# Performance work log

Hardware: AMD Instinct MI355X
Metric: run time of the kernel (lower is better)

## Reference

```python
import jax, jax.numpy as jnp
import numpy as np

N = 262144          # nodes
E = N * 16          # edges (avg degree 16)
C_IN = 64
C_OUT = 64
GRID = 0.5          # voxel size
POS_EXTENT = 10.0   # pos in [0, 10)^3
NVOX_DIM = int(round(POS_EXTENT / GRID))  # 20
NVOX = NVOX_DIM ** 3                      # 8000 voxels
BN_EPS = 1e-5


def setup_inputs() -> dict:
    key = jax.random.key(0)
    k = jax.random.split(key, 5)
    x = jax.random.normal(k[0], (N, C_IN), dtype=jnp.float32)
    pos = jax.random.uniform(k[1], (N, 3), dtype=jnp.float32, minval=0.0, maxval=POS_EXTENT)
    edge_index = jax.random.randint(k[2], (2, E), 0, N, dtype=jnp.int32)
    W = jax.random.normal(k[3], (C_IN, C_OUT), dtype=jnp.float32) / np.float32(np.sqrt(C_IN))
    b = jnp.zeros((C_OUT,), jnp.float32)
    gamma = jnp.ones((C_OUT,), jnp.float32)
    beta = jnp.zeros((C_OUT,), jnp.float32)
    return {"x": x, "pos": pos, "edge_index": edge_index,
            "W": W, "b": b, "gamma": gamma, "beta": beta}


def reference(x, pos, edge_index, W, b, gamma, beta):
    # --- self.down: Linear -> BatchNorm1d (training-mode batch stats) -> ReLU ---
    h = x @ W + b                                   # [N, C_OUT]
    mean = jnp.mean(h, axis=0)
    var = jnp.mean(jnp.square(h - mean), axis=0)    # biased variance (torch BN)
    h = (h - mean) * jax.lax.rsqrt(var + BN_EPS) * gamma + beta
    h = jax.nn.relu(h)

    # --- max_pool_neighbor_x: scatter-max of neighbor features (self-loops added) ---
    row, col = edge_index[0], edge_index[1]
    pooled = jax.ops.segment_max(h[row], col, num_segments=N)  # [N, C_OUT]
    h = jnp.maximum(pooled, h)  # self-loop; also fixes -inf for isolated nodes

    # --- GridSampling: voxel-grid quantize + per-voxel mean of x and pos ---
    vid = jnp.clip(jnp.floor(pos / GRID).astype(jnp.int32), 0, NVOX_DIM - 1)  # [N,3]
    vox = (vid[:, 0] * NVOX_DIM + vid[:, 1]) * NVOX_DIM + vid[:, 2]           # [N]
    cnt = jax.ops.segment_sum(jnp.ones((N,), jnp.float32), vox, num_segments=NVOX)
    x_sum = jax.ops.segment_sum(h, vox, num_segments=NVOX)     # [NVOX, C_OUT]
    p_sum = jax.ops.segment_sum(pos, vox, num_segments=NVOX)   # [NVOX, 3]
    denom = jnp.maximum(cnt, 1.0)[:, None]
    x_out = x_sum / denom
    pos_out = p_sum / denom
    # concat features and positions of the downsampled graph: [NVOX, C_OUT+3]
    return jnp.concatenate([x_out, pos_out], axis=1)
```

## Files before the change

kernel.cpp:

```cpp
#include <hip/hip_runtime.h>
#include <hip/hip_fp16.h>

#define NVOX_DIM 20
#define NVOX 8000
#define BN_EPS 1e-5f

#define NBUCK 1024
#define BSHIFT 8
#define NODES_PER_BUCK 256
#define GEMM_BLOCKS 1024
#define XTRA_BLOCKS 64
#define CAP_NEW 8192
#define CAP_OLD 5120
#define VCAP 88
#define CSTRIDE 16
#define VSTRIDE 4

typedef _Float16 f16x8 __attribute__((ext_vector_type(8)));
typedef float f32x4 __attribute__((ext_vector_type(4)));

__device__ __forceinline__ unsigned short f2key(float v) {
    unsigned short hb = __half_as_ushort(__float2half(v));
    unsigned short m = (unsigned short)(0x8000u | (unsigned short)(-(int)(hb >> 15)));
    return (unsigned short)(hb ^ m);
}

__device__ __forceinline__ float key2f(unsigned int k) {
    unsigned short hb = (k & 0x8000u) ? (unsigned short)(k ^ 0x8000u)
                                      : (unsigned short)(0xFFFFu ^ k);
    __half_raw hr;
    hr.x = hb;
    return __half2float((__half)hr);
}

__global__ __launch_bounds__(256) void k_zero(int* __restrict__ p, int n) {
    int i = blockIdx.x * 256 + threadIdx.x;
    if (i < n) p[i] = 0;
}

template <int NEW>
__global__ __launch_bounds__(256) void k0_fused(const float* __restrict__ x,
                                                const float* __restrict__ W,
                                                const float* __restrict__ bias,
                                                unsigned short* __restrict__ h16,
                                                float* __restrict__ partials, int n16,
                                                const int* __restrict__ rows,
                                                const int* __restrict__ cols,
                                                int* __restrict__ cursor,
                                                unsigned int* __restrict__ pairs,
                                                const float* __restrict__ pos,
                                                int* __restrict__ vcursor,
                                                int* __restrict__ vlist,
                                                float4* __restrict__ zero_zone,
                                                int zero_n4) {
    __shared__ float sW[4096];
    __shared__ float red[2][4][64];
    __shared__ int lh[NBUCK];
    __shared__ int lpos[NBUCK];
    const int cap = NEW ? CAP_NEW : CAP_OLD;
    int t = threadIdx.x;
    int bid = blockIdx.x;

    if (bid >= 2 * GEMM_BLOCKS) {
        int zb = bid - 2 * GEMM_BLOCKS;
        if (NEW) {
            int nNodes = n16 * 16;
            for (int nd = zb * 256 + t; nd < nNodes; nd += XTRA_BLOCKS * 256) {
                float px = pos[(size_t)nd * 3 + 0];
                float py = pos[(size_t)nd * 3 + 1];
                float pz = pos[(size_t)nd * 3 + 2];
                int v0 = min(max((int)floorf(px * 2.f), 0), NVOX_DIM - 1);
                int v1 = min(max((int)floorf(py * 2.f), 0), NVOX_DIM - 1);
                int v2 = min(max((int)floorf(pz * 2.f), 0), NVOX_DIM - 1);
                int vox = (v0 * NVOX_DIM + v1) * NVOX_DIM + v2;
                int idx = atomicAdd(&vcursor[vox * VSTRIDE], 1);
                if (idx < VCAP) vlist[vox * VCAP + idx] = nd;
            }
        } else {
            float4 z = {0.f, 0.f, 0.f, 0.f};
            for (int i = zb * 256 + t; i < zero_n4; i += XTRA_BLOCKS * 256) zero_zone[i] = z;
        }
        return;
    }

    if (bid & 1) {
        int bb = bid >> 1;
        for (int j = t; j < NBUCK; j += 256) lh[j] = 0;
        __syncthreads();
        int base = bb * 4096 + t * 16;
        int r[16], c[16];
#pragma unroll
        for (int g4 = 0; g4 < 4; ++g4) {
            int e = base + g4 * 4;
            int4 r4 = *(const int4*)(rows + e);
            int4 c4 = *(const int4*)(cols + e);
            r[g4 * 4 + 0] = r4.x; c[g4 * 4 + 0] = c4.x;
            r[g4 * 4 + 1] = r4.y; c[g4 * 4 + 1] = c4.y;
            r[g4 * 4 + 2] = r4.z; c[g4 * 4 + 2] = c4.z;
            r[g4 * 4 + 3] = r4.w; c[g4 * 4 + 3] = c4.w;
        }
#pragma unroll
        for (int i = 0; i < 16; ++i) atomicAdd(&lh[c[i] >> BSHIFT], 1);
        __syncthreads();
        for (int j = t; j < NBUCK; j += 256)
            lpos[j] = atomicAdd(&cursor[j * (NEW ? CSTRIDE : 1)], lh[j]);
        __syncthreads();
#pragma unroll
        for (int i = 0; i < 16; ++i) {
            int bkt = c[i] >> BSHIFT;
            int idx = atomicAdd(&lpos[bkt], 1);
            if (idx < cap)
                pairs[(size_t)bkt * cap + idx] =
                    ((unsigned int)r[i] << 8) | (unsigned int)(c[i] & (NODES_PER_BUCK - 1));
        }
        return;
    }

    int gb = bid >> 1;
    for (int i = t; i < 4096; i += 256) sW[i] = W[i];
    __syncthreads();
    int lane = t & 63;
    int w = t >> 6;
    int l15 = lane & 15;
    int q = lane >> 4;

    f16x8 bf[4][2];
#pragma unroll
    for (int t4 = 0; t4 < 4; ++t4)
#pragma unroll
        for (int kb = 0; kb < 2; ++kb)
#pragma unroll
            for (int i = 0; i < 8; ++i)
                bf[t4][kb][i] = (_Float16)sW[(kb * 32 + q * 8 + i) * 64 + t4 * 16 + l15];
    float bv[4];
#pragma unroll
    for (int t4 = 0; t4 < 4; ++t4) bv[t4] = bias[t4 * 16 + l15];

    float s[4] = {0.f, 0.f, 0.f, 0.f}, s2[4] = {0.f, 0.f, 0.f, 0.f};

    for (int g = gb * 4 + w; g < n16; g += GEMM_BLOCKS * 4) {
        int row0 = g * 16;
        const float* xp = x + (size_t)(row0 + l15) * 64 + q * 8;
        float4 xa = *(const float4*)(xp);
        float4 xb = *(const float4*)(xp + 4);
        float4 xc = *(const float4*)(xp + 32);
        float4 xd = *(const float4*)(xp + 36);
        f16x8 a0, a1;
        a0[0] = (_Float16)xa.x; a0[1] = (_Float16)xa.y; a0[2] = (_Float16)xa.z; a0[3] = (_Float16)xa.w;
        a0[4] = (_Float16)xb.x; a0[5] = (_Float16)xb.y; a0[6] = (_Float16)xb.z; a0[7] = (_Float16)xb.w;
        a1[0] = (_Float16)xc.x; a1[1] = (_Float16)xc.y; a1[2] = (_Float16)xc.z; a1[3] = (_Float16)xc.w;
        a1[4] = (_Float16)xd.x; a1[5] = (_Float16)xd.y; a1[6] = (_Float16)xd.z; a1[7] = (_Float16)xd.w;

#pragma unroll
        for (int t4 = 0; t4 < 4; ++t4) {
            f32x4 acc = {bv[t4], bv[t4], bv[t4], bv[t4]};
            acc = __builtin_amdgcn_mfma_f32_16x16x32_f16(a0, bf[t4][0], acc, 0, 0, 0);
            acc = __builtin_amdgcn_mfma_f32_16x16x32_f16(a1, bf[t4][1], acc, 0, 0, 0);
            s[t4] += acc[0] + acc[1] + acc[2] + acc[3];
            s2[t4] = fmaf(acc[0], acc[0], s2[t4]);
            s2[t4] = fmaf(acc[1], acc[1], s2[t4]);
            s2[t4] = fmaf(acc[2], acc[2], s2[t4]);
            s2[t4] = fmaf(acc[3], acc[3], s2[t4]);
#pragma unroll
            for (int r = 0; r < 4; ++r) {
                h16[(size_t)(row0 + q * 4 + r) * 64 + t4 * 16 + l15] = f2key(acc[r]);
            }
        }
    }

#pragma unroll
    for (int t4 = 0; t4 < 4; ++t4) {
        s[t4] += __shfl_xor(s[t4], 16, 64);
        s[t4] += __shfl_xor(s[t4], 32, 64);
        s2[t4] += __shfl_xor(s2[t4], 16, 64);
        s2[t4] += __shfl_xor(s2[t4], 32, 64);
    }
    if (lane < 16) {
#pragma unroll
        for (int t4 = 0; t4 < 4; ++t4) {
            red[0][w][t4 * 16 + lane] = s[t4];
            red[1][w][t4 * 16 + lane] = s2[t4];
        }
    }
    __syncthreads();
    if (t < 128) {
        int c = t & 63;
        int which = t >> 6;
        float v = red[which][0][c] + red[which][1][c] + red[which][2][c] + red[which][3][c];
        partials[(size_t)gb * 128 + which * 64 + c] = v;
    }
}

__global__ __launch_bounds__(1024) void k3_finalize(const float* __restrict__ partials,
                                                    const float* __restrict__ gamma,
                                                    const float* __restrict__ beta,
                                                    float* __restrict__ stats2, float invN) {
    __shared__ float red[8][128];
    __shared__ float tot[128];
    int t = threadIdx.x;
    int c = t & 127;
    int g = t >> 7;
    float s = 0.f;
    for (int b = g; b < GEMM_BLOCKS; b += 8) s += partials[(size_t)b * 128 + c];
    red[g][c] = s;
    __syncthreads();
    if (t < 128) {
        float v = 0.f;
#pragma unroll
        for (int g2 = 0; g2 < 8; ++g2) v += red[g2][t];
        tot[t] = v;
    }
    __syncthreads();
    if (t < 64) {
        float mean = tot[t] * invN;
        float var = tot[64 + t] * invN - mean * mean;
        float sc = gamma[t] * rsqrtf(var + BN_EPS);
        stats2[t] = sc;
        stats2[64 + t] = beta[t] - mean * sc;
    }
}

template <int NEW>
__global__ __launch_bounds__(1024) void k_pool(const unsigned int* pairs_,
                                               const int* __restrict__ cursor,
                                               const unsigned short* __restrict__ h16,
                                               const float* __restrict__ pos,
                                               float* __restrict__ stats2,
                                               float* __restrict__ xs,
                                               float* __restrict__ ps,
                                               float* __restrict__ cnt,
                                               unsigned short* pooled16,
                                               const float* __restrict__ partials,
                                               const float* __restrict__ gamma,
                                               const float* __restrict__ beta,
                                               float invN) {
    __shared__ unsigned int tile[NODES_PER_BUCK * 64];
    const int cap = NEW ? CAP_NEW : CAP_OLD;
    int b = blockIdx.x;
    int t = threadIdx.x;

    if (NEW && b == NBUCK) {
        float* fred = (float*)tile;
        float* tot = ((float*)tile) + 1024;
        int c = t & 127;
        int g = t >> 7;
        float s = 0.f;
        for (int pb = g; pb < GEMM_BLOCKS; pb += 8) s += partials[(size_t)pb * 128 + c];
        fred[g * 128 + c] = s;
        __syncthreads();
        if (t < 128) {
            float v = 0.f;
#pragma unroll
            for (int g2 = 0; g2 < 8; ++g2) v += fred[g2 * 128 + t];
            tot[t] = v;
        }
        __syncthreads();
        if (t < 64) {
            float mean = tot[t] * invN;
            float var = tot[64 + t] * invN - mean * mean;
            float sc = gamma[t] * rsqrtf(var + BN_EPS);
            stats2[t] = sc;
            stats2[64 + t] = beta[t] - mean * sc;
        }
        return;
    }

    int lane = t & 63;
    int w = t >> 6;

    const unsigned int* src = (const unsigned int*)(h16 + (size_t)b * (NODES_PER_BUCK * 64));
#pragma unroll
    for (int k = 0; k < 8; ++k) {
        int i = t + k * 1024;
        unsigned int u = src[i];
        tile[2 * i] = u & 0xFFFFu;
        tile[2 * i + 1] = u >> 16;
    }
    __syncthreads();

    int cntE = min(cursor[b * (NEW ? CSTRIDE : 1)], cap);
    int start = b * cap;
    int end = start + cntE;
    int chunk = (cntE + 15) >> 4;
    int cs = start + w * chunk;
    int ce = min(cs + chunk, end);
    for (int j0 = cs; j0 < ce; j0 += 64) {
        int lim = min(64, ce - j0);
        unsigned int pk = (lane < lim) ? pairs_[j0 + lane] : 0u;
        int jj = 0;
        for (; jj + 16 <= lim; jj += 16) {
            unsigned int qv[16];
            unsigned short vv[16];
#pragma unroll
            for (int u = 0; u < 16; ++u)
                qv[u] = (unsigned int)__builtin_amdgcn_readlane((int)pk, jj + u);
#pragma unroll
            for (int u = 0; u < 16; ++u) vv[u] = h16[(size_t)(qv[u] >> 8) * 64 + lane];
#pragma unroll
            for (int u = 0; u < 16; ++u)
                atomicMax(&tile[((qv[u] & 255u) << 6) + lane], (unsigned int)vv[u]);
        }
        for (; jj < lim; ++jj) {
            unsigned int qq = (unsigned int)__builtin_amdgcn_readlane((int)pk, jj);
            unsigned int v = h16[(size_t)(qq >> 8) * 64 + lane];
            atomicMax(&tile[((qq & 255u) << 6) + lane], v);
        }
    }
    __syncthreads();

    if (NEW) {
#pragma unroll
        for (int nl = 0; nl < NODES_PER_BUCK; nl += 16) {
            int node_l = nl + w;
            pooled16[((size_t)((b << BSHIFT) + node_l)) * 64 + lane] =
                (unsigned short)tile[(node_l << 6) + lane];
        }
    } else {
        float scale = stats2[lane];
        float shift = stats2[64 + lane];
#pragma unroll
        for (int nl = 0; nl < NODES_PER_BUCK; nl += 16) {
            int node_l = nl + w;
            int c = (b << BSHIFT) + node_l;
            float px = pos[(size_t)c * 3 + 0];
            float py = pos[(size_t)c * 3 + 1];
            float pz = pos[(size_t)c * 3 + 2];
            int v0 = min(max((int)floorf(px * 2.f), 0), NVOX_DIM - 1);
            int v1 = min(max((int)floorf(py * 2.f), 0), NVOX_DIM - 1);
            int v2 = min(max((int)floorf(pz * 2.f), 0), NVOX_DIM - 1);
            int vox = (v0 * NVOX_DIM + v1) * NVOX_DIM + v2;
            float v = key2f(tile[(node_l << 6) + lane]);
            float val = fmaxf(fmaf(v, scale, shift), 0.f);
            atomicAdd(&xs[(size_t)vox * 64 + lane], val);
            if (lane < 3) atomicAdd(&ps[vox * 3 + lane], lane == 0 ? px : (lane == 1 ? py : pz));
            if (lane == 0) atomicAdd(&cnt[vox], 1.f);
        }
    }
}

__global__ __launch_bounds__(256) void k_vox(const unsigned short* __restrict__ pooled16,
                                             const int* __restrict__ vlist,
                                             const int* __restrict__ vcursor,
                                             const float* __restrict__ pos,
                                             const float* __restrict__ stats2,
                                             float* __restrict__ out) {
    int v = blockIdx.x * 4 + (threadIdx.x >> 6);
    int lane = threadIdx.x & 63;
    int cv = vcursor[v * VSTRIDE];
    int c = min(cv, VCAP);
    float scale = stats2[lane], shift = stats2[64 + lane];
    const int* lst = vlist + (size_t)v * VCAP;
    float s0 = 0.f, s1 = 0.f, s2 = 0.f, s3 = 0.f;
    int i = 0;
    for (; i + 4 <= c; i += 4) {
        int n0 = lst[i], n1 = lst[i + 1], n2 = lst[i + 2], n3 = lst[i + 3];
        float v0 = key2f(pooled16[(size_t)n0 * 64 + lane]);
        float v1 = key2f(pooled16[(size_t)n1 * 64 + lane]);
        float v2 = key2f(pooled16[(size_t)n2 * 64 + lane]);
        float v3 = key2f(pooled16[(size_t)n3 * 64 + lane]);
        s0 += fmaxf(fmaf(v0, scale, shift), 0.f);
        s1 += fmaxf(fmaf(v1, scale, shift), 0.f);
        s2 += fmaxf(fmaf(v2, scale, shift), 0.f);
        s3 += fmaxf(fmaf(v3, scale, shift), 0.f);
    }
    for (; i < c; ++i) {
        float v0 = key2f(pooled16[(size_t)lst[i] * 64 + lane]);
        s0 += fmaxf(fmaf(v0, scale, shift), 0.f);
    }
    float den = 1.f / fmaxf((float)cv, 1.f);
    out[(size_t)v * 67 + lane] = (s0 + s1 + s2 + s3) * den;
    if (lane < 3) {
        float p0 = 0.f, p1 = 0.f, p2 = 0.f, p3 = 0.f;
        int j = 0;
        for (; j + 4 <= c; j += 4) {
            p0 += pos[(size_t)lst[j] * 3 + lane];
            p1 += pos[(size_t)lst[j + 1] * 3 + lane];
            p2 += pos[(size_t)lst[j + 2] * 3 + lane];
            p3 += pos[(size_t)lst[j + 3] * 3 + lane];
        }
        for (; j < c; ++j) p0 += pos[(size_t)lst[j] * 3 + lane];
        out[(size_t)v * 67 + 64 + lane] = (p0 + p1 + p2 + p3) * den;
    }
}

__global__ __launch_bounds__(256) void k7_out(const float* __restrict__ xs,
                                              const float* __restrict__ ps,
                                              const float* __restrict__ cnt,
                                              float* __restrict__ out, int total) {
    int idx = blockIdx.x * blockDim.x + threadIdx.x;
    if (idx >= total) return;
    int v = idx / 67;
    int c = idx - v * 67;
    float d = fmaxf(cnt[v], 1.f);
    float val = (c < 64) ? xs[(size_t)v * 64 + c] : ps[v * 3 + (c - 64)];
    out[idx] = val / d;
}

extern "C" void kernel_launch(void* const* d_in, const int* in_sizes, int n_in,
                              void* d_out, int out_size, void* d_ws, size_t ws_size,
                              hipStream_t stream) {
    const float* x     = (const float*)d_in[0];
    const float* pos   = (const float*)d_in[1];
    const int*   ei    = (const int*)d_in[2];
    const float* W     = (const float*)d_in[3];
    const float* b     = (const float*)d_in[4];
    const float* gamma = (const float*)d_in[5];
    const float* beta  = (const float*)d_in[6];
    float* out = (float*)d_out;

    const int n = in_sizes[0] / 64;
    const int E = in_sizes[2] / 2;
    char* ws = (char*)d_ws;

    const size_t NEED_NEW = 70643712;
    if (ws_size >= NEED_NEW) {
        unsigned short* h16      = (unsigned short*)(ws + 0);
        unsigned int*   pairs    = (unsigned int*)(ws + 33554432);
        unsigned short* pooled16 = (unsigned short*)(ws + 33554432);
        float*          partials = (float*)(ws + 67108864);
        float*          stats2   = (float*)(ws + 67633152);
        int*            cursor   = (int*)(ws + 67634176);
        int*            vcursor  = (int*)(ws + 67699712);
        int*            vlist    = (int*)(ws + 67827712);

        k_zero<<<189, 256, 0, stream>>>(cursor, 48384);
        k0_fused<1><<<2 * GEMM_BLOCKS + XTRA_BLOCKS, 256, 0, stream>>>(
            x, W, b, h16, partials, n >> 4, ei, ei + E, cursor, pairs,
            pos, vcursor, vlist, nullptr, 0);
        k_pool<1><<<NBUCK + 1, 1024, 0, stream>>>(pairs, cursor, h16, nullptr, stats2,
                                                  nullptr, nullptr, nullptr, pooled16,
                                                  partials, gamma, beta, 1.0f / (float)n);
        k_vox<<<NVOX / 4, 256, 0, stream>>>(pooled16, vlist, vcursor, pos, stats2, out);
    } else {
        unsigned short* h16      = (unsigned short*)(ws + 0);
        unsigned int*   pairs    = (unsigned int*)(ws + 33554432);
        float*          partials = (float*)(ws + 54525952);
        float*          stats2   = (float*)(ws + 55050240);
        int*            cursor   = (int*)(ws + 55051264);
        float*          xs       = (float*)(ws + 55055360);
        float*          ps       = (float*)(ws + 57103360);
        float*          cnt      = (float*)(ws + 57199360);
        float4*         zero4    = (float4*)(ws + 55055360);
        const int zero_n4 = (57231360 - 55055360) / 16;

        k_zero<<<4, 256, 0, stream>>>(cursor, NBUCK);
        k0_fused<0><<<2 * GEMM_BLOCKS + XTRA_BLOCKS, 256, 0, stream>>>(
            x, W, b, h16, partials, n >> 4, ei, ei + E, cursor, pairs,
            nullptr, nullptr, nullptr, zero4, zero_n4);
        k3_finalize<<<1, 1024, 0, stream>>>(partials, gamma, beta, stats2, 1.0f / (float)n);
        k_pool<0><<<NBUCK, 1024, 0, stream>>>(pairs, cursor, h16, pos, stats2,
                                              xs, ps, cnt, nullptr, nullptr, nullptr,
                                              nullptr, 0.f);
        k7_out<<<(out_size + 255) / 256, 256, 0, stream>>>(xs, ps, cnt, out, out_size);
    }
}
```

Before: 322.1 us.

## Replace LDS atomicMax pooling with per-bucket counting sort and register max

The default-path pooling kernel now sorts each bucket's edges by destination node using an LDS histogram, a wave scan and a scatter into a compact edge list. Each wave then reduces its nodes' neighbour features in registers with unsigned max, and the self-loop value is folded in. This removes the 64 KB LDS tile and the per-edge LDS atomics and cuts LDS use a lot, which should allow better occupancy. In exchange there is an extra pass over the pairs. Edges beyond ELCAP (4608) per bucket are silently dropped, which risks correctness under skewed degree distributions. The old path is kept as a separate non-template kernel.

```diff
diff --git a/kernel.cpp b/kernel.cpp
--- a/kernel.cpp
+++ b/kernel.cpp
@@ -12,12 +12,17 @@
 #define XTRA_BLOCKS 64
 #define CAP_NEW 8192
 #define CAP_OLD 5120
+#define ELCAP 4608
 #define VCAP 88
 #define CSTRIDE 16
 #define VSTRIDE 4
 
 typedef _Float16 f16x8 __attribute__((ext_vector_type(8)));
 typedef float f32x4 __attribute__((ext_vector_type(4)));
+
+__device__ __forceinline__ unsigned int umaxu(unsigned int a, unsigned int b) {
+    return a > b ? a : b;
+}
 
 __device__ __forceinline__ unsigned short f2key(float v) {
     unsigned short hb = __half_as_ushort(__float2half(v));
@@ -220,28 +225,25 @@
     }
 }
 
-template <int NEW>
-__global__ __launch_bounds__(1024) void k_pool(const unsigned int* pairs_,
-                                               const int* __restrict__ cursor,
-                                               const unsigned short* __restrict__ h16,
-                                               const float* __restrict__ pos,
-                                               float* __restrict__ stats2,
-                                               float* __restrict__ xs,
-                                               float* __restrict__ ps,
-                                               float* __restrict__ cnt,
-                                               unsigned short* pooled16,
-                                               const float* __restrict__ partials,
-                                               const float* __restrict__ gamma,
-                                               const float* __restrict__ beta,
-                                               float invN) {
-    __shared__ unsigned int tile[NODES_PER_BUCK * 64];
-    const int cap = NEW ? CAP_NEW : CAP_OLD;
+__global__ __launch_bounds__(1024) void k_pool2(const unsigned int* __restrict__ pairs_,
+                                                const int* __restrict__ cursor,
+                                                const unsigned short* __restrict__ h16,
+                                                float* __restrict__ stats2,
+                                                unsigned short* __restrict__ pooled16,
+                                                const float* __restrict__ partials,
+                                                const float* __restrict__ gamma,
+                                                const float* __restrict__ beta,
+                                                float invN) {
+    __shared__ int cnt[NODES_PER_BUCK];
+    __shared__ int off[NODES_PER_BUCK];
+    __shared__ int wpos[NODES_PER_BUCK];
+    __shared__ unsigned int elist[ELCAP];
     int b = blockIdx.x;
     int t = threadIdx.x;
 
-    if (NEW && b == NBUCK) {
-        float* fred = (float*)tile;
-        float* tot = ((float*)tile) + 1024;
+    if (b == NBUCK) {
+        float* fred = (float*)elist;
+        float* tot = ((float*)elist) + 1024;
         int c = t & 127;
         int g = t >> 7;
         float s = 0.f;
@@ -268,6 +270,94 @@
     int lane = t & 63;
     int w = t >> 6;
 
+    if (t < NODES_PER_BUCK) cnt[t] = 0;
+    __syncthreads();
+
+    int cntE = min(cursor[b * CSTRIDE], ELCAP);
+    size_t start = (size_t)b * CAP_NEW;
+
+    for (int e = t; e < cntE; e += 1024) atomicAdd(&cnt[pairs_[start + e] & 255u], 1);
+    __syncthreads();
+
+    if (t < 64) {
+        int c0 = cnt[4 * t], c1 = cnt[4 * t + 1], c2 = cnt[4 * t + 2], c3 = cnt[4 * t + 3];
+        int p = c0 + c1 + c2 + c3;
+        int inc = p;
+        for (int d = 1; d < 64; d <<= 1) {
+            int v = __shfl_up(inc, d, 64);
+            if (t >= d) inc += v;
+        }
+        int base = inc - p;
+        off[4 * t] = base;               wpos[4 * t] = base;
+        off[4 * t + 1] = base + c0;      wpos[4 * t + 1] = base + c0;
+        off[4 * t + 2] = base + c0 + c1; wpos[4 * t + 2] = base + c0 + c1;
+        off[4 * t + 3] = base + c0 + c1 + c2; wpos[4 * t + 3] = base + c0 + c1 + c2;
+    }
+    __syncthreads();
+
+    for (int e = t; e < cntE; e += 1024) {
+        unsigned int pk = pairs_[start + e];
+        int idx = atomicAdd(&wpos[pk & 255u], 1);
+        elist[idx] = pk >> 8;
+    }
+    __syncthreads();
+
+#pragma unroll
+    for (int i = 0; i < NODES_PER_BUCK / 16; ++i) {
+        int node = w * 16 + i;
+        int gnode = (b << BSHIFT) + node;
+        unsigned int reg = (unsigned int)h16[(size_t)gnode * 64 + lane];
+        int n = cnt[node];
+        int base = off[node];
+        for (int j0 = 0; j0 < n; j0 += 64) {
+            int m = min(64, n - j0);
+            unsigned int el = (lane < m) ? elist[base + j0 + lane] : 0u;
+            int e = 0;
+            for (; e + 8 <= m; e += 8) {
+                int r0 = __builtin_amdgcn_readlane((int)el, e);
+                int r1 = __builtin_amdgcn_readlane((int)el, e + 1);
+                int r2 = __builtin_amdgcn_readlane((int)el, e + 2);
+                int r3 = __builtin_amdgcn_readlane((int)el, e + 3);
+                int r4 = __builtin_amdgcn_readlane((int)el, e + 4);
+                int r5 = __builtin_amdgcn_readlane((int)el, e + 5);
+                int r6 = __builtin_amdgcn_readlane((int)el, e + 6);
+                int r7 = __builtin_amdgcn_readlane((int)el, e + 7);
+                unsigned int v0 = h16[(size_t)r0 * 64 + lane];
+                unsigned int v1 = h16[(size_t)r1 * 64 + lane];
+                unsigned int v2 = h16[(size_t)r2 * 64 + lane];
+                unsigned int v3 = h16[(size_t)r3 * 64 + lane];
+                unsigned int v4 = h16[(size_t)r4 * 64 + lane];
+                unsigned int v5 = h16[(size_t)r5 * 64 + lane];
+                unsigned int v6 = h16[(size_t)r6 * 64 + lane];
+                unsigned int v7 = h16[(size_t)r7 * 64 + lane];
+                reg = umaxu(reg, umaxu(umaxu(umaxu(v0, v1), umaxu(v2, v3)),
+                                       umaxu(umaxu(v4, v5), umaxu(v6, v7))));
+            }
+            for (; e < m; ++e) {
+                int r0 = __builtin_amdgcn_readlane((int)el, e);
+                reg = umaxu(reg, (unsigned int)h16[(size_t)r0 * 64 + lane]);
+            }
+        }
+        pooled16[(size_t)gnode * 64 + lane] = (unsigned short)reg;
+    }
+}
+
+__global__ __launch_bounds__(1024) void k_pool(const unsigned int* __restrict__ pairs_,
+                                               const int* __restrict__ cursor,
+                                               const unsigned short* __restrict__ h16,
+                                               const float* __restrict__ pos,
+                                               const float* __restrict__ stats2,
+                                               float* __restrict__ xs,
+                                               float* __restrict__ ps,
+                                               float* __restrict__ cnt) {
+    __shared__ unsigned int tile[NODES_PER_BUCK * 64];
+    int b = blockIdx.x;
+    int t = threadIdx.x;
+    int lane = t & 63;
+    int w = t >> 6;
+    float scale = stats2[lane];
+    float shift = stats2[64 + lane];
+
     const unsigned int* src = (const unsigned int*)(h16 + (size_t)b * (NODES_PER_BUCK * 64));
 #pragma unroll
     for (int k = 0; k < 8; ++k) {
@@ -278,8 +368,8 @@
     }
     __syncthreads();
 
-    int cntE = min(cursor[b * (NEW ? CSTRIDE : 1)], cap);
-    int start = b * cap;
+    int cntE = min(cursor[b], CAP_OLD);
+    int start = b * CAP_OLD;
     int end = start + cntE;
     int chunk = (cntE + 15) >> 4;
     int cs = start + w * chunk;
@@ -308,33 +398,22 @@
     }
     __syncthreads();
 
-    if (NEW) {
-#pragma unroll
-        for (int nl = 0; nl < NODES_PER_BUCK; nl += 16) {
-            int node_l = nl + w;
-            pooled16[((size_t)((b << BSHIFT) + node_l)) * 64 + lane] =
-                (unsigned short)tile[(node_l << 6) + lane];
-        }
-    } else {
-        float scale = stats2[lane];
-        float shift = stats2[64 + lane];
-#pragma unroll
-        for (int nl = 0; nl < NODES_PER_BUCK; nl += 16) {
-            int node_l = nl + w;
-            int c = (b << BSHIFT) + node_l;
-            float px = pos[(size_t)c * 3 + 0];
-            float py = pos[(size_t)c * 3 + 1];
-            float pz = pos[(size_t)c * 3 + 2];
-            int v0 = min(max((int)floorf(px * 2.f), 0), NVOX_DIM - 1);
-            int v1 = min(max((int)floorf(py * 2.f), 0), NVOX_DIM - 1);
-            int v2 = min(max((int)floorf(pz * 2.f), 0), NVOX_DIM - 1);
-            int vox = (v0 * NVOX_DIM + v1) * NVOX_DIM + v2;
-            float v = key2f(tile[(node_l << 6) + lane]);
-            float val = fmaxf(fmaf(v, scale, shift), 0.f);
-            atomicAdd(&xs[(size_t)vox * 64 + lane], val);
-            if (lane < 3) atomicAdd(&ps[vox * 3 + lane], lane == 0 ? px : (lane == 1 ? py : pz));
-            if (lane == 0) atomicAdd(&cnt[vox], 1.f);
-        }
+#pragma unroll
+    for (int nl = 0; nl < NODES_PER_BUCK; nl += 16) {
+        int node_l = nl + w;
+        int c = (b << BSHIFT) + node_l;
+        float px = pos[(size_t)c * 3 + 0];
+        float py = pos[(size_t)c * 3 + 1];
+        float pz = pos[(size_t)c * 3 + 2];
+        int v0 = min(max((int)floorf(px * 2.f), 0), NVOX_DIM - 1);
+        int v1 = min(max((int)floorf(py * 2.f), 0), NVOX_DIM - 1);
+        int v2 = min(max((int)floorf(pz * 2.f), 0), NVOX_DIM - 1);
+        int vox = (v0 * NVOX_DIM + v1) * NVOX_DIM + v2;
+        float v = key2f(tile[(node_l << 6) + lane]);
+        float val = fmaxf(fmaf(v, scale, shift), 0.f);
+        atomicAdd(&xs[(size_t)vox * 64 + lane], val);
+        if (lane < 3) atomicAdd(&ps[vox * 3 + lane], lane == 0 ? px : (lane == 1 ? py : pz));
+        if (lane == 0) atomicAdd(&cnt[vox], 1.f);
     }
 }
 
@@ -427,9 +506,8 @@
         k0_fused<1><<<2 * GEMM_BLOCKS + XTRA_BLOCKS, 256, 0, stream>>>(
             x, W, b, h16, partials, n >> 4, ei, ei + E, cursor, pairs,
             pos, vcursor, vlist, nullptr, 0);
-        k_pool<1><<<NBUCK + 1, 1024, 0, stream>>>(pairs, cursor, h16, nullptr, stats2,
-                                                  nullptr, nullptr, nullptr, pooled16,
-                                                  partials, gamma, beta, 1.0f / (float)n);
+        k_pool2<<<NBUCK + 1, 1024, 0, stream>>>(pairs, cursor, h16, stats2, pooled16,
+                                                partials, gamma, beta, 1.0f / (float)n);
         k_vox<<<NVOX / 4, 256, 0, stream>>>(pooled16, vlist, vcursor, pos, stats2, out);
     } else {
         unsigned short* h16      = (unsigned short*)(ws + 0);
@@ -448,9 +526,7 @@
             x, W, b, h16, partials, n >> 4, ei, ei + E, cursor, pairs,
             nullptr, nullptr, nullptr, zero4, zero_n4);
         k3_finalize<<<1, 1024, 0, stream>>>(partials, gamma, beta, stats2, 1.0f / (float)n);
-        k_pool<0><<<NBUCK, 1024, 0, stream>>>(pairs, cursor, h16, pos, stats2,
-                                              xs, ps, cnt, nullptr, nullptr, nullptr,
-                                              nullptr, 0.f);
+        k_pool<<<NBUCK, 1024, 0, stream>>>(pairs, cursor, h16, pos, stats2, xs, ps, cnt);
         k7_out<<<(out_size + 255) / 256, 256, 0, stream>>>(xs, ps, cnt, out, out_size);
     }
 }
```

New measurement: 351.0 us. +9.0%, slower.

## Split edge binning into separate kernel with shared-memory staged coalesced writes

Applied to the files above, without the earlier changes.

Edge bucketing moves out of the fused GEMM kernel into its own kernel. Each 1024-thread block bins 16384 edges, prefix-sums the bucket histogram, stages the packed pairs in LDS sorted by bucket, then writes each bucket's run contiguously to global memory. This replaces the scattered per-edge global stores with more coalesced writes. The cost is an extra launch and the loss of overlap between GEMM and binning, which previously ran in one grid; the fallback path is only split into non-templated kernels.

```diff
diff --git a/kernel.cpp b/kernel.cpp
--- a/kernel.cpp
+++ b/kernel.cpp
@@ -15,6 +15,7 @@
 #define VCAP 88
 #define CSTRIDE 16
 #define VSTRIDE 4
+#define BIN_EPB 16384
 
 typedef _Float16 f16x8 __attribute__((ext_vector_type(8)));
 typedef float f32x4 __attribute__((ext_vector_type(4)));
@@ -38,85 +39,37 @@
     if (i < n) p[i] = 0;
 }
 
-template <int NEW>
-__global__ __launch_bounds__(256) void k0_fused(const float* __restrict__ x,
-                                                const float* __restrict__ W,
-                                                const float* __restrict__ bias,
-                                                unsigned short* __restrict__ h16,
-                                                float* __restrict__ partials, int n16,
-                                                const int* __restrict__ rows,
-                                                const int* __restrict__ cols,
-                                                int* __restrict__ cursor,
-                                                unsigned int* __restrict__ pairs,
-                                                const float* __restrict__ pos,
-                                                int* __restrict__ vcursor,
-                                                int* __restrict__ vlist,
-                                                float4* __restrict__ zero_zone,
-                                                int zero_n4) {
+__global__ __launch_bounds__(256) void k0_gemm(const float* __restrict__ x,
+                                               const float* __restrict__ W,
+                                               const float* __restrict__ bias,
+                                               unsigned short* __restrict__ h16,
+                                               float* __restrict__ partials, int n16,
+                                               const float* __restrict__ pos,
+                                               int* __restrict__ vcursor,
+                                               int* __restrict__ vlist) {
     __shared__ float sW[4096];
     __shared__ float red[2][4][64];
-    __shared__ int lh[NBUCK];
-    __shared__ int lpos[NBUCK];
-    const int cap = NEW ? CAP_NEW : CAP_OLD;
     int t = threadIdx.x;
     int bid = blockIdx.x;
 
-    if (bid >= 2 * GEMM_BLOCKS) {
-        int zb = bid - 2 * GEMM_BLOCKS;
-        if (NEW) {
-            int nNodes = n16 * 16;
-            for (int nd = zb * 256 + t; nd < nNodes; nd += XTRA_BLOCKS * 256) {
-                float px = pos[(size_t)nd * 3 + 0];
-                float py = pos[(size_t)nd * 3 + 1];
-                float pz = pos[(size_t)nd * 3 + 2];
-                int v0 = min(max((int)floorf(px * 2.f), 0), NVOX_DIM - 1);
-                int v1 = min(max((int)floorf(py * 2.f), 0), NVOX_DIM - 1);
-                int v2 = min(max((int)floorf(pz * 2.f), 0), NVOX_DIM - 1);
-                int vox = (v0 * NVOX_DIM + v1) * NVOX_DIM + v2;
-                int idx = atomicAdd(&vcursor[vox * VSTRIDE], 1);
-                if (idx < VCAP) vlist[vox * VCAP + idx] = nd;
-            }
-        } else {
-            float4 z = {0.f, 0.f, 0.f, 0.f};
-            for (int i = zb * 256 + t; i < zero_n4; i += XTRA_BLOCKS * 256) zero_zone[i] = z;
+    if (bid >= GEMM_BLOCKS) {
+        int zb = bid - GEMM_BLOCKS;
+        int nNodes = n16 * 16;
+        for (int nd = zb * 256 + t; nd < nNodes; nd += XTRA_BLOCKS * 256) {
+            float px = pos[(size_t)nd * 3 + 0];
+            float py = pos[(size_t)nd * 3 + 1];
+            float pz = pos[(size_t)nd * 3 + 2];
+            int v0 = min(max((int)floorf(px * 2.f), 0), NVOX_DIM - 1);
+            int v1 = min(max((int)floorf(py * 2.f), 0), NVOX_DIM - 1);
+            int v2 = min(max((int)floorf(pz * 2.f), 0), NVOX_DIM - 1);
+            int vox = (v0 * NVOX_DIM + v1) * NVOX_DIM + v2;
+            int idx = atomicAdd(&vcursor[vox * VSTRIDE], 1);
+            if (idx < VCAP) vlist[vox * VCAP + idx] = nd;
         }
         return;
     }
 
-    if (bid & 1) {
-        int bb = bid >> 1;
-        for (int j = t; j < NBUCK; j += 256) lh[j] = 0;
-        __syncthreads();
-        int base = bb * 4096 + t * 16;
-        int r[16], c[16];
-#pragma unroll
-        for (int g4 = 0; g4 < 4; ++g4) {
-            int e = base + g4 * 4;
-            int4 r4 = *(const int4*)(rows + e);
-            int4 c4 = *(const int4*)(cols + e);
-            r[g4 * 4 + 0] = r4.x; c[g4 * 4 + 0] = c4.x;
-            r[g4 * 4 + 1] = r4.y; c[g4 * 4 + 1] = c4.y;
-            r[g4 * 4 + 2] = r4.z; c[g4 * 4 + 2] = c4.z;
-            r[g4 * 4 + 3] = r4.w; c[g4 * 4 + 3] = c4.w;
-        }
-#pragma unroll
-        for (int i = 0; i < 16; ++i) atomicAdd(&lh[c[i] >> BSHIFT], 1);
-        __syncthreads();
-        for (int j = t; j < NBUCK; j += 256)
-            lpos[j] = atomicAdd(&cursor[j * (NEW ? CSTRIDE : 1)], lh[j]);
-        __syncthreads();
-#pragma unroll
-        for (int i = 0; i < 16; ++i) {
-            int bkt = c[i] >> BSHIFT;
-            int idx = atomicAdd(&lpos[bkt], 1);
-            if (idx < cap)
-                pairs[(size_t)bkt * cap + idx] =
-                    ((unsigned int)r[i] << 8) | (unsigned int)(c[i] & (NODES_PER_BUCK - 1));
-        }
-        return;
-    }
-
-    int gb = bid >> 1;
+    int gb = bid;
     for (int i = t; i < 4096; i += 256) sW[i] = W[i];
     __syncthreads();
     int lane = t & 63;
@@ -191,55 +144,87 @@
     }
 }
 
-__global__ __launch_bounds__(1024) void k3_finalize(const float* __restrict__ partials,
-                                                    const float* __restrict__ gamma,
-                                                    const float* __restrict__ beta,
-                                                    float* __restrict__ stats2, float invN) {
-    __shared__ float red[8][128];
-    __shared__ float tot[128];
+__global__ __launch_bounds__(1024) void k_bin2(const int* __restrict__ rows,
+                                               const int* __restrict__ cols,
+                                               int* __restrict__ cursor,
+                                               unsigned int* __restrict__ pairs) {
+    __shared__ unsigned int buf[BIN_EPB];
+    __shared__ int hist[NBUCK];
+    __shared__ int wpos[NBUCK];
+    __shared__ int gbase[NBUCK];
+    __shared__ int wsum[16];
     int t = threadIdx.x;
-    int c = t & 127;
-    int g = t >> 7;
-    float s = 0.f;
-    for (int b = g; b < GEMM_BLOCKS; b += 8) s += partials[(size_t)b * 128 + c];
-    red[g][c] = s;
-    __syncthreads();
-    if (t < 128) {
-        float v = 0.f;
-#pragma unroll
-        for (int g2 = 0; g2 < 8; ++g2) v += red[g2][t];
-        tot[t] = v;
-    }
-    __syncthreads();
-    if (t < 64) {
-        float mean = tot[t] * invN;
-        float var = tot[64 + t] * invN - mean * mean;
-        float sc = gamma[t] * rsqrtf(var + BN_EPS);
-        stats2[t] = sc;
-        stats2[64 + t] = beta[t] - mean * sc;
-    }
-}
-
-template <int NEW>
-__global__ __launch_bounds__(1024) void k_pool(const unsigned int* pairs_,
-                                               const int* __restrict__ cursor,
-                                               const unsigned short* __restrict__ h16,
-                                               const float* __restrict__ pos,
-                                               float* __restrict__ stats2,
-                                               float* __restrict__ xs,
-                                               float* __restrict__ ps,
-                                               float* __restrict__ cnt,
-                                               unsigned short* pooled16,
-                                               const float* __restrict__ partials,
-                                               const float* __restrict__ gamma,
-                                               const float* __restrict__ beta,
-                                               float invN) {
+    int lane = t & 63;
+    int w = t >> 6;
+
+    hist[t] = 0;
+    __syncthreads();
+
+    int base_e = blockIdx.x * BIN_EPB + t * 16;
+    int r[16], c[16];
+#pragma unroll
+    for (int g4 = 0; g4 < 4; ++g4) {
+        int e = base_e + g4 * 4;
+        int4 r4 = *(const int4*)(rows + e);
+        int4 c4 = *(const int4*)(cols + e);
+        r[g4 * 4 + 0] = r4.x; c[g4 * 4 + 0] = c4.x;
+        r[g4 * 4 + 1] = r4.y; c[g4 * 4 + 1] = c4.y;
+        r[g4 * 4 + 2] = r4.z; c[g4 * 4 + 2] = c4.z;
+        r[g4 * 4 + 3] = r4.w; c[g4 * 4 + 3] = c4.w;
+    }
+#pragma unroll
+    for (int i = 0; i < 16; ++i) atomicAdd(&hist[c[i] >> BSHIFT], 1);
+    __syncthreads();
+
+    int v = hist[t];
+    int inc = v;
+    for (int d = 1; d < 64; d <<= 1) {
+        int u = __shfl_up(inc, d, 64);
+        if (lane >= d) inc += u;
+    }
+    if (lane == 63) wsum[w] = inc;
+    __syncthreads();
+    int add = 0;
+    for (int ww = 0; ww < w; ++ww) add += wsum[ww];
+    wpos[t] = inc - v + add;
+    gbase[t] = atomicAdd(&cursor[t * CSTRIDE], v);
+    __syncthreads();
+
+#pragma unroll
+    for (int i = 0; i < 16; ++i) {
+        int bkt = c[i] >> BSHIFT;
+        int idx = atomicAdd(&wpos[bkt], 1);
+        buf[idx] = ((unsigned int)r[i] << 8) | (unsigned int)(c[i] & (NODES_PER_BUCK - 1));
+    }
+    __syncthreads();
+
+    for (int it = 0; it < NBUCK / 16 / 4; ++it) {  }
+    for (int it = 0; it < 64; ++it) {
+        int j = w * 64 + it;
+        int cnt = hist[j];
+        int src = wpos[j] - cnt;
+        int dst0 = gbase[j];
+        for (int k2 = lane; k2 < cnt; k2 += 64) {
+            int d = dst0 + k2;
+            if (d < CAP_NEW) pairs[(size_t)j * CAP_NEW + d] = buf[src + k2];
+        }
+    }
+}
+
+__global__ __launch_bounds__(1024) void k_pool_new(const unsigned int* __restrict__ pairs_,
+                                                   const int* __restrict__ cursor,
+                                                   const unsigned short* __restrict__ h16,
+                                                   float* __restrict__ stats2,
+                                                   unsigned short* __restrict__ pooled16,
+                                                   const float* __restrict__ partials,
+                                                   const float* __restrict__ gamma,
+                                                   const float* __restrict__ beta,
+                                                   float invN) {
     __shared__ unsigned int tile[NODES_PER_BUCK * 64];
-    const int cap = NEW ? CAP_NEW : CAP_OLD;
     int b = blockIdx.x;
     int t = threadIdx.x;
 
-    if (NEW && b == NBUCK) {
+    if (b == NBUCK) {
         float* fred = (float*)tile;
         float* tot = ((float*)tile) + 1024;
         int c = t & 127;
@@ -278,8 +263,8 @@
     }
     __syncthreads();
 
-    int cntE = min(cursor[b * (NEW ? CSTRIDE : 1)], cap);
-    int start = b * cap;
+    int cntE = min(cursor[b * CSTRIDE], CAP_NEW);
+    int start = b * CAP_NEW;
     int end = start + cntE;
     int chunk = (cntE + 15) >> 4;
     int cs = start + w * chunk;
@@ -308,33 +293,11 @@
     }
     __syncthreads();
 
-    if (NEW) {
-#pragma unroll
-        for (int nl = 0; nl < NODES_PER_BUCK; nl += 16) {
-            int node_l = nl + w;
-            pooled16[((size_t)((b << BSHIFT) + node_l)) * 64 + lane] =
-                (unsigned short)tile[(node_l << 6) + lane];
-        }
-    } else {
-        float scale = stats2[lane];
-        float shift = stats2[64 + lane];
-#pragma unroll
-        for (int nl = 0; nl < NODES_PER_BUCK; nl += 16) {
-            int node_l = nl + w;
-            int c = (b << BSHIFT) + node_l;
-            float px = pos[(size_t)c * 3 + 0];
-            float py = pos[(size_t)c * 3 + 1];
-            float pz = pos[(size_t)c * 3 + 2];
-            int v0 = min(max((int)floorf(px * 2.f), 0), NVOX_DIM - 1);
-            int v1 = min(max((int)floorf(py * 2.f), 0), NVOX_DIM - 1);
-            int v2 = min(max((int)floorf(pz * 2.f), 0), NVOX_DIM - 1);
-            int vox = (v0 * NVOX_DIM + v1) * NVOX_DIM + v2;
-            float v = key2f(tile[(node_l << 6) + lane]);
-            float val = fmaxf(fmaf(v, scale, shift), 0.f);
-            atomicAdd(&xs[(size_t)vox * 64 + lane], val);
-            if (lane < 3) atomicAdd(&ps[vox * 3 + lane], lane == 0 ? px : (lane == 1 ? py : pz));
-            if (lane == 0) atomicAdd(&cnt[vox], 1.f);
-        }
+#pragma unroll
+    for (int nl = 0; nl < NODES_PER_BUCK; nl += 16) {
+        int node_l = nl + w;
+        pooled16[((size_t)((b << BSHIFT) + node_l)) * 64 + lane] =
+            (unsigned short)tile[(node_l << 6) + lane];
     }
 }
 
@@ -383,6 +346,242 @@
     }
 }
 
+__global__ __launch_bounds__(256) void k0_fused_old(const float* __restrict__ x,
+                                                    const float* __restrict__ W,
+                                                    const float* __restrict__ bias,
+                                                    unsigned short* __restrict__ h16,
+                                                    float* __restrict__ partials, int n16,
+                                                    const int* __restrict__ rows,
+                                                    const int* __restrict__ cols,
+                                                    int* __restrict__ cursor,
+                                                    unsigned int* __restrict__ pairs,
+                                                    float4* __restrict__ zero_zone,
+                                                    int zero_n4) {
+    __shared__ float sW[4096];
+    __shared__ float red[2][4][64];
+    __shared__ int lh[NBUCK];
+    __shared__ int lpos[NBUCK];
+    int t = threadIdx.x;
+    int bid = blockIdx.x;
+
+    if (bid >= 2 * GEMM_BLOCKS) {
+        int zb = bid - 2 * GEMM_BLOCKS;
+        float4 z = {0.f, 0.f, 0.f, 0.f};
+        for (int i = zb * 256 + t; i < zero_n4; i += XTRA_BLOCKS * 256) zero_zone[i] = z;
+        return;
+    }
+
+    if (bid & 1) {
+        int bb = bid >> 1;
+        for (int j = t; j < NBUCK; j += 256) lh[j] = 0;
+        __syncthreads();
+        int base = bb * 4096 + t * 16;
+        int r[16], c[16];
+#pragma unroll
+        for (int g4 = 0; g4 < 4; ++g4) {
+            int e = base + g4 * 4;
+            int4 r4 = *(const int4*)(rows + e);
+            int4 c4 = *(const int4*)(cols + e);
+            r[g4 * 4 + 0] = r4.x; c[g4 * 4 + 0] = c4.x;
+            r[g4 * 4 + 1] = r4.y; c[g4 * 4 + 1] = c4.y;
+            r[g4 * 4 + 2] = r4.z; c[g4 * 4 + 2] = c4.z;
+            r[g4 * 4 + 3] = r4.w; c[g4 * 4 + 3] = c4.w;
+        }
+#pragma unroll
+        for (int i = 0; i < 16; ++i) atomicAdd(&lh[c[i] >> BSHIFT], 1);
+        __syncthreads();
+        for (int j = t; j < NBUCK; j += 256) lpos[j] = atomicAdd(&cursor[j], lh[j]);
+        __syncthreads();
+#pragma unroll
+        for (int i = 0; i < 16; ++i) {
+            int bkt = c[i] >> BSHIFT;
+            int idx = atomicAdd(&lpos[bkt], 1);
+            if (idx < CAP_OLD)
+                pairs[(size_t)bkt * CAP_OLD + idx] =
+                    ((unsigned int)r[i] << 8) | (unsigned int)(c[i] & (NODES_PER_BUCK - 1));
+        }
+        return;
+    }
+
+    int gb = bid >> 1;
+    for (int i = t; i < 4096; i += 256) sW[i] = W[i];
+    __syncthreads();
+    int lane = t & 63;
+    int w = t >> 6;
+    int l15 = lane & 15;
+    int q = lane >> 4;
+
+    f16x8 bf[4][2];
+#pragma unroll
+    for (int t4 = 0; t4 < 4; ++t4)
+#pragma unroll
+        for (int kb = 0; kb < 2; ++kb)
+#pragma unroll
+            for (int i = 0; i < 8; ++i)
+                bf[t4][kb][i] = (_Float16)sW[(kb * 32 + q * 8 + i) * 64 + t4 * 16 + l15];
+    float bv[4];
+#pragma unroll
+    for (int t4 = 0; t4 < 4; ++t4) bv[t4] = bias[t4 * 16 + l15];
+
+    float s[4] = {0.f, 0.f, 0.f, 0.f}, s2[4] = {0.f, 0.f, 0.f, 0.f};
+
+    for (int g = gb * 4 + w; g < n16; g += GEMM_BLOCKS * 4) {
+        int row0 = g * 16;
+        const float* xp = x + (size_t)(row0 + l15) * 64 + q * 8;
+        float4 xa = *(const float4*)(xp);
+        float4 xb = *(const float4*)(xp + 4);
+        float4 xc = *(const float4*)(xp + 32);
+        float4 xd = *(const float4*)(xp + 36);
+        f16x8 a0, a1;
+        a0[0] = (_Float16)xa.x; a0[1] = (_Float16)xa.y; a0[2] = (_Float16)xa.z; a0[3] = (_Float16)xa.w;
+        a0[4] = (_Float16)xb.x; a0[5] = (_Float16)xb.y; a0[6] = (_Float16)xb.z; a0[7] = (_Float16)xb.w;
+        a1[0] = (_Float16)xc.x; a1[1] = (_Float16)xc.y; a1[2] = (_Float16)xc.z; a1[3] = (_Float16)xc.w;
+        a1[4] = (_Float16)xd.x; a1[5] = (_Float16)xd.y; a1[6] = (_Float16)xd.z; a1[7] = (_Float16)xd.w;
+
+#pragma unroll
+        for (int t4 = 0; t4 < 4; ++t4) {
+            f32x4 acc = {bv[t4], bv[t4], bv[t4], bv[t4]};
+            acc = __builtin_amdgcn_mfma_f32_16x16x32_f16(a0, bf[t4][0], acc, 0, 0, 0);
+            acc = __builtin_amdgcn_mfma_f32_16x16x32_f16(a1, bf[t4][1], acc, 0, 0, 0);
+            s[t4] += acc[0] + acc[1] + acc[2] + acc[3];
+            s2[t4] = fmaf(acc[0], acc[0], s2[t4]);
+            s2[t4] = fmaf(acc[1], acc[1], s2[t4]);
+            s2[t4] = fmaf(acc[2], acc[2], s2[t4]);
+            s2[t4] = fmaf(acc[3], acc[3], s2[t4]);
+#pragma unroll
+            for (int r = 0; r < 4; ++r) {
+                h16[(size_t)(row0 + q * 4 + r) * 64 + t4 * 16 + l15] = f2key(acc[r]);
+            }
+        }
+    }
+
+#pragma unroll
+    for (int t4 = 0; t4 < 4; ++t4) {
+        s[t4] += __shfl_xor(s[t4], 16, 64);
+        s[t4] += __shfl_xor(s[t4], 32, 64);
+        s2[t4] += __shfl_xor(s2[t4], 16, 64);
+        s2[t4] += __shfl_xor(s2[t4], 32, 64);
+    }
+    if (lane < 16) {
+#pragma unroll
+        for (int t4 = 0; t4 < 4; ++t4) {
+            red[0][w][t4 * 16 + lane] = s[t4];
+            red[1][w][t4 * 16 + lane] = s2[t4];
+        }
+    }
+    __syncthreads();
+    if (t < 128) {
+        int c = t & 63;
+        int which = t >> 6;
+        float v = red[which][0][c] + red[which][1][c] + red[which][2][c] + red[which][3][c];
+        partials[(size_t)gb * 128 + which * 64 + c] = v;
+    }
+}
+
+__global__ __launch_bounds__(1024) void k3_finalize(const float* __restrict__ partials,
+                                                    const float* __restrict__ gamma,
+                                                    const float* __restrict__ beta,
+                                                    float* __restrict__ stats2, float invN) {
+    __shared__ float red[8][128];
+    __shared__ float tot[128];
+    int t = threadIdx.x;
+    int c = t & 127;
+    int g = t >> 7;
+    float s = 0.f;
+    for (int b = g; b < GEMM_BLOCKS; b += 8) s += partials[(size_t)b * 128 + c];
+    red[g][c] = s;
+    __syncthreads();
+    if (t < 128) {
+        float v = 0.f;
+#pragma unroll
+        for (int g2 = 0; g2 < 8; ++g2) v += red[g2][t];
+        tot[t] = v;
+    }
+    __syncthreads();
+    if (t < 64) {
+        float mean = tot[t] * invN;
+        float var = tot[64 + t] * invN - mean * mean;
+        float sc = gamma[t] * rsqrtf(var + BN_EPS);
+        stats2[t] = sc;
+        stats2[64 + t] = beta[t] - mean * sc;
+    }
+}
+
+__global__ __launch_bounds__(1024) void k_pool_old(const unsigned int* __restrict__ pairs_,
+                                                   const int* __restrict__ cursor,
+                                                   const unsigned short* __restrict__ h16,
+                                                   const float* __restrict__ pos,
+                                                   const float* __restrict__ stats2,
+                                                   float* __restrict__ xs,
+                                                   float* __restrict__ ps,
+                                                   float* __restrict__ cnt) {
+    __shared__ unsigned int tile[NODES_PER_BUCK * 64];
+    int b = blockIdx.x;
+    int t = threadIdx.x;
+    int lane = t & 63;
+    int w = t >> 6;
+    float scale = stats2[lane];
+    float shift = stats2[64 + lane];
+
+    const unsigned int* src = (const unsigned int*)(h16 + (size_t)b * (NODES_PER_BUCK * 64));
+#pragma unroll
+    for (int k = 0; k < 8; ++k) {
+        int i = t + k * 1024;
+        unsigned int u = src[i];
+        tile[2 * i] = u & 0xFFFFu;
+        tile[2 * i + 1] = u >> 16;
+    }
+    __syncthreads();
+
+    int cntE = min(cursor[b], CAP_OLD);
+    int start = b * CAP_OLD;
+    int end = start + cntE;
+    int chunk = (cntE + 15) >> 4;
+    int cs = start + w * chunk;
+    int ce = min(cs + chunk, end);
+    for (int j0 = cs; j0 < ce; j0 += 64) {
+        int lim = min(64, ce - j0);
+        unsigned int pk = (lane < lim) ? pairs_[j0 + lane] : 0u;
+        int jj = 0;
+        for (; jj + 16 <= lim; jj += 16) {
+            unsigned int qv[16];
+            unsigned short vv[16];
+#pragma unroll
+            for (int u = 0; u < 16; ++u)
+                qv[u] = (unsigned int)__builtin_amdgcn_readlane((int)pk, jj + u);
+#pragma unroll
+            for (int u = 0; u < 16; ++u) vv[u] = h16[(size_t)(qv[u] >> 8) * 64 + lane];
+#pragma unroll
+            for (int u = 0; u < 16; ++u)
+                atomicMax(&tile[((qv[u] & 255u) << 6) + lane], (unsigned int)vv[u]);
+        }
+        for (; jj < lim; ++jj) {
+            unsigned int qq = (unsigned int)__builtin_amdgcn_readlane((int)pk, jj);
+            unsigned int v = h16[(size_t)(qq >> 8) * 64 + lane];
+            atomicMax(&tile[((qq & 255u) << 6) + lane], v);
+        }
+    }
+    __syncthreads();
+
+#pragma unroll
+    for (int nl = 0; nl < NODES_PER_BUCK; nl += 16) {
+        int node_l = nl + w;
+        int c = (b << BSHIFT) + node_l;
+        float px = pos[(size_t)c * 3 + 0];
+        float py = pos[(size_t)c * 3 + 1];
+        float pz = pos[(size_t)c * 3 + 2];
+        int v0 = min(max((int)floorf(px * 2.f), 0), NVOX_DIM - 1);
+        int v1 = min(max((int)floorf(py * 2.f), 0), NVOX_DIM - 1);
+        int v2 = min(max((int)floorf(pz * 2.f), 0), NVOX_DIM - 1);
+        int vox = (v0 * NVOX_DIM + v1) * NVOX_DIM + v2;
+        float v = key2f(tile[(node_l << 6) + lane]);
+        float val = fmaxf(fmaf(v, scale, shift), 0.f);
+        atomicAdd(&xs[(size_t)vox * 64 + lane], val);
+        if (lane < 3) atomicAdd(&ps[vox * 3 + lane], lane == 0 ? px : (lane == 1 ? py : pz));
+        if (lane == 0) atomicAdd(&cnt[vox], 1.f);
+    }
+}
+
 __global__ __launch_bounds__(256) void k7_out(const float* __restrict__ xs,
                                               const float* __restrict__ ps,
                                               const float* __restrict__ cnt,
@@ -424,12 +623,11 @@
         int*            vlist    = (int*)(ws + 67827712);
 
         k_zero<<<189, 256, 0, stream>>>(cursor, 48384);
-        k0_fused<1><<<2 * GEMM_BLOCKS + XTRA_BLOCKS, 256, 0, stream>>>(
-            x, W, b, h16, partials, n >> 4, ei, ei + E, cursor, pairs,
-            pos, vcursor, vlist, nullptr, 0);
-        k_pool<1><<<NBUCK + 1, 1024, 0, stream>>>(pairs, cursor, h16, nullptr, stats2,
-                                                  nullptr, nullptr, nullptr, pooled16,
-                                                  partials, gamma, beta, 1.0f / (float)n);
+        k0_gemm<<<GEMM_BLOCKS + XTRA_BLOCKS, 256, 0, stream>>>(
+            x, W, b, h16, partials, n >> 4, pos, vcursor, vlist);
+        k_bin2<<<E / BIN_EPB, 1024, 0, stream>>>(ei, ei + E, cursor, pairs);
+        k_pool_new<<<NBUCK + 1, 1024, 0, stream>>>(pairs, cursor, h16, stats2, pooled16,
+                                                   partials, gamma, beta, 1.0f / (float)n);
         k_vox<<<NVOX / 4, 256, 0, stream>>>(pooled16, vlist, vcursor, pos, stats2, out);
     } else {
         unsigned short* h16      = (unsigned short*)(ws + 0);
@@ -444,13 +642,10 @@
         const int zero_n4 = (57231360 - 55055360) / 16;
 
         k_zero<<<4, 256, 0, stream>>>(cursor, NBUCK);
-        k0_fused<0><<<2 * GEMM_BLOCKS + XTRA_BLOCKS, 256, 0, stream>>>(
-            x, W, b, h16, partials, n >> 4, ei, ei + E, cursor, pairs,
-            nullptr, nullptr, nullptr, zero4, zero_n4);
+        k0_fused_old<<<2 * GEMM_BLOCKS + XTRA_BLOCKS, 256, 0, stream>>>(
+            x, W, b, h16, partials, n >> 4, ei, ei + E, cursor, pairs, zero4, zero_n4);
         k3_finalize<<<1, 1024, 0, stream>>>(partials, gamma, beta, stats2, 1.0f / (float)n);
-        k_pool<0><<<NBUCK, 1024, 0, stream>>>(pairs, cursor, h16, pos, stats2,
-                                              xs, ps, cnt, nullptr, nullptr, nullptr,
-                                              nullptr, 0.f);
+        k_pool_old<<<NBUCK, 1024, 0, stream>>>(pairs, cursor, h16, pos, stats2, xs, ps, cnt);
         k7_out<<<(out_size + 255) / 256, 256, 0, stream>>>(xs, ps, cnt, out, out_size);
     }
 }
```

Result: no change. 323.6 us (+0.5%).
